# Kernel tuning notes

Hardware: AMD Instinct MI355X
Metric: run time of the kernel (lower is better)

Reference implementation:

```python
import jax, jax.numpy as jnp
import numpy as np

B, S, HID = 2, 2048, 3072
NH, NKV, HD = 16, 8, 256
N_REP = NH // NKV
BITS, BLK = 4, 128
THETA = 10000.0
NEG = -1e9


def quantize_bfp(x, bits=BITS, block_size=BLK):
    """Block-floating-point quantization: blocks of `block_size` along the last
    (head_dim) axis share one power-of-two exponent; mantissas get `bits` levels
    (sign + bits-1), round-to-nearest."""
    shape = x.shape
    xb = x.reshape(-1, block_size)
    maxabs = jnp.max(jnp.abs(xb), axis=-1, keepdims=True)
    e = jnp.floor(jnp.log2(jnp.maximum(maxabs, 1e-30)))
    scale = jnp.exp2(e - (bits - 2))  # largest mantissa ~ 2^(bits-1)-1 covers maxabs
    qmax = 2.0 ** (bits - 1) - 1.0
    q = jnp.clip(jnp.round(xb / scale), -qmax, qmax) * scale
    q = jnp.where(maxabs > 0, q, 0.0)
    return q.reshape(shape)


def rotate_half(x):
    x1, x2 = jnp.split(x, 2, axis=-1)
    return jnp.concatenate((-x2, x1), axis=-1)


def setup_inputs() -> dict:
    key = jax.random.key(0)
    ks = jax.random.split(key, 5)
    hidden_states = jax.random.normal(ks[0], (B, S, HID), dtype=jnp.float32)
    sd = 0.02
    Wq = jax.random.normal(ks[1], (NH * HD, HID), dtype=jnp.float32) * sd
    Wk = jax.random.normal(ks[2], (NKV * HD, HID), dtype=jnp.float32) * sd
    Wv = jax.random.normal(ks[3], (NKV * HD, HID), dtype=jnp.float32) * sd
    Wo = jax.random.normal(ks[4], (HID, NH * HD), dtype=jnp.float32) * sd
    # rotary tables (HF convention: concat(freqs, freqs))
    pos = jnp.arange(S, dtype=jnp.float32)
    inv_freq = 1.0 / (THETA ** (jnp.arange(0, HD, 2, dtype=jnp.float32) / HD))
    freqs = jnp.einsum('s,d->sd', pos, inv_freq)
    emb = jnp.concatenate((freqs, freqs), axis=-1)  # (S, HD)
    cos = jnp.cos(emb)[None]  # (1, S, HD)
    sin = jnp.sin(emb)[None]
    # additive causal mask (B, 1, S, S)
    causal = jnp.where(jnp.tril(jnp.ones((S, S), dtype=bool)), 0.0, NEG).astype(jnp.float32)
    attention_mask = jnp.broadcast_to(causal[None, None], (B, 1, S, S))
    return {"hidden_states": hidden_states, "Wq": Wq, "Wk": Wk, "Wv": Wv,
            "Wo": Wo, "cos": cos, "sin": sin, "attention_mask": attention_mask}


def reference(hidden_states, Wq, Wk, Wv, Wo, cos, sin, attention_mask):
    b, s, _ = hidden_states.shape
    q = jnp.einsum('bsh,dh->bsd', hidden_states, Wq).reshape(b, s, NH, HD).transpose(0, 2, 1, 3)
    k = jnp.einsum('bsh,dh->bsd', hidden_states, Wk).reshape(b, s, NKV, HD).transpose(0, 2, 1, 3)
    v = jnp.einsum('bsh,dh->bsd', hidden_states, Wv).reshape(b, s, NKV, HD).transpose(0, 2, 1, 3)
    # RoPE (cos/sin unsqueezed at dim 1 -> (1,1,S,HD))
    c, sn = cos[:, None], sin[:, None]
    q = q * c + rotate_half(q) * sn
    k = k * c + rotate_half(k) * sn
    # int4 BFP quantization of keys (along rows of head_dim)
    k = quantize_bfp(k)
    # GQA: repeat kv heads
    k = jnp.repeat(k, N_REP, axis=1)
    v = jnp.repeat(v, N_REP, axis=1)
    scores = jnp.einsum('bhqd,bhkd->bhqk', q, k) / jnp.sqrt(jnp.float32(HD))
    scores = scores + attention_mask
    attn = jax.nn.softmax(scores.astype(jnp.float32), axis=-1).astype(q.dtype)
    out = jnp.einsum('bhqk,bhkd->bhqd', attn, v)
    out = out.transpose(0, 2, 1, 3).reshape(b, s, NH * HD)
    return jnp.einsum('bsd,hd->bsh', out, Wo)
```

## Files before the change

### kernel.cpp

```cpp
#include <hip/hip_runtime.h>
#include <math.h>

#define Bsz 2
#define Ssz 2048
#define HIDs 3072
#define NHs 16
#define NKVs 8
#define HDs 256

typedef _Float16 f16;
typedef _Float16 f16x8 __attribute__((ext_vector_type(8)));
typedef _Float16 f16x4 __attribute__((ext_vector_type(4)));
typedef float f32x4 __attribute__((ext_vector_type(4)));

__device__ __forceinline__ void async16(const f16* g, f16* l) {
    __builtin_amdgcn_global_load_lds(
        (const __attribute__((address_space(1))) void*)g,
        (__attribute__((address_space(3))) void*)l, 16, 0, 0);
}

__device__ __forceinline__ float row_max16(float v) {
    int t;
    t = __builtin_amdgcn_mov_dpp(__float_as_int(v), 0x121, 0xf, 0xf, false);
    v = fmaxf(v, __int_as_float(t));
    t = __builtin_amdgcn_mov_dpp(__float_as_int(v), 0x122, 0xf, 0xf, false);
    v = fmaxf(v, __int_as_float(t));
    t = __builtin_amdgcn_mov_dpp(__float_as_int(v), 0x124, 0xf, 0xf, false);
    v = fmaxf(v, __int_as_float(t));
    t = __builtin_amdgcn_mov_dpp(__float_as_int(v), 0x128, 0xf, 0xf, false);
    v = fmaxf(v, __int_as_float(t));
    return v;
}
__device__ __forceinline__ float row_sum16(float v) {
    int t;
    t = __builtin_amdgcn_mov_dpp(__float_as_int(v), 0x121, 0xf, 0xf, false);
    v = v + __int_as_float(t);
    t = __builtin_amdgcn_mov_dpp(__float_as_int(v), 0x122, 0xf, 0xf, false);
    v = v + __int_as_float(t);
    t = __builtin_amdgcn_mov_dpp(__float_as_int(v), 0x124, 0xf, 0xf, false);
    v = v + __int_as_float(t);
    t = __builtin_amdgcn_mov_dpp(__float_as_int(v), 0x128, 0xf, 0xf, false);
    v = v + __int_as_float(t);
    return v;
}

__global__ void cast_f32_f16_v4(const float4* __restrict__ in, f16x4* __restrict__ out, int n4) {
    int i = blockIdx.x * blockDim.x + threadIdx.x;
    if (i < n4) {
        float4 v = in[i];
        f16x4 r;
        r[0] = (f16)v.x; r[1] = (f16)v.y; r[2] = (f16)v.z; r[3] = (f16)v.w;
        out[i] = r;
    }
}

__global__ __launch_bounds__(256) void gemm_nt_f16(
    const f16* __restrict__ A, const f16* __restrict__ Bm, float* __restrict__ C,
    int M, int N, int K)
{
    __shared__ __align__(16) f16 As[128 * 32];
    __shared__ __align__(16) f16 Bs[128 * 32];
    const int tid  = threadIdx.x;
    const int wave = tid >> 6, lane = tid & 63;
    const int l15  = lane & 15, quad = lane >> 4;
    const int m0 = blockIdx.y * 128, n0 = blockIdx.x * 128;
    const int wm = (wave >> 1) * 64, wn = (wave & 1) * 64;
    const int srow = wave * 32 + (lane >> 2);
    const int scol = (lane & 3) * 8;

    f32x4 acc[4][4];
    const f32x4 fz = {0.f, 0.f, 0.f, 0.f};
#pragma unroll
    for (int i = 0; i < 4; i++)
#pragma unroll
        for (int j = 0; j < 4; j++) acc[i][j] = fz;

    const f16* Ag0 = A  + (size_t)(m0 + srow) * K + scol;
    const f16* Ag1 = A  + (size_t)(m0 + srow + 16) * K + scol;
    const f16* Bg0 = Bm + (size_t)(n0 + srow) * K + scol;
    const f16* Bg1 = Bm + (size_t)(n0 + srow + 16) * K + scol;
    f16* Al0 = As + (wave * 32) * 32;
    f16* Al1 = As + (wave * 32 + 16) * 32;
    f16* Bl0 = Bs + (wave * 32) * 32;
    f16* Bl1 = Bs + (wave * 32 + 16) * 32;

    for (int k0 = 0; k0 < K; k0 += 32) {
        __syncthreads();
        async16(Ag0 + k0, Al0);
        async16(Ag1 + k0, Al1);
        async16(Bg0 + k0, Bl0);
        async16(Bg1 + k0, Bl1);
        __syncthreads();
        f16x8 af[4], bfr[4];
#pragma unroll
        for (int i = 0; i < 4; i++)
            af[i] = *(const f16x8*)(As + (wm + i * 16 + l15) * 32 + quad * 8);
#pragma unroll
        for (int j = 0; j < 4; j++)
            bfr[j] = *(const f16x8*)(Bs + (wn + j * 16 + l15) * 32 + quad * 8);
#pragma unroll
        for (int i = 0; i < 4; i++)
#pragma unroll
            for (int j = 0; j < 4; j++)
                acc[i][j] = __builtin_amdgcn_mfma_f32_16x16x32_f16(af[i], bfr[j], acc[i][j], 0, 0, 0);
    }
#pragma unroll
    for (int i = 0; i < 4; i++) {
        const int r = m0 + wm + i * 16 + quad * 4;
#pragma unroll
        for (int j = 0; j < 4; j++) {
            const int c = n0 + wn + j * 16 + l15;
#pragma unroll
            for (int rr = 0; rr < 4; rr++)
                C[(size_t)(r + rr) * N + c] = acc[i][j][rr];
        }
    }
}

__global__ void rope_q_kernel(const float* __restrict__ qp, const float* __restrict__ cosb,
                              const float* __restrict__ sinb, f16* __restrict__ qo) {
    const int s = blockIdx.x, h = blockIdx.y, b = blockIdx.z;
    const int d = threadIdx.x;
    const float* row = qp + (size_t)(b * Ssz + s) * (NHs * HDs) + h * HDs;
    float x = row[d];
    float other = (d < 128) ? -row[d + 128] : row[d - 128];
    float val = (x * cosb[s * HDs + d] + other * sinb[s * HDs + d]) * 0.0625f;
    qo[((size_t)(b * NHs + h) * Ssz + s) * HDs + d] = (f16)val;
}

__global__ void rope_quant_k_kernel(const float* __restrict__ kp, const float* __restrict__ cosb,
                                    const float* __restrict__ sinb, f16* __restrict__ ko) {
    const int s = blockIdx.x, h = blockIdx.y, b = blockIdx.z;
    const int d = threadIdx.x;
    const float* row = kp + (size_t)(b * Ssz + s) * (NKVs * HDs) + h * HDs;
    float x = row[d];
    float other = (d < 128) ? -row[d + 128] : row[d - 128];
    float val = x * cosb[s * HDs + d] + other * sinb[s * HDs + d];
    __shared__ float red[256];
    red[d] = fabsf(val);
    __syncthreads();
    for (int off = 64; off >= 1; off >>= 1) {
        if ((d & 127) < off) red[d] = fmaxf(red[d], red[d + off]);
        __syncthreads();
    }
    float maxabs = red[d & 128];
    float out;
    if (maxabs > 0.f) {
        int ex;
        frexpf(maxabs, &ex);
        float scale = ldexpf(1.0f, ex - 3);
        float q = rintf(val / scale);
        q = fminf(7.f, fmaxf(-7.f, q));
        out = q * scale;
    } else out = 0.f;
    ko[((size_t)(b * NKVs + h) * Ssz + s) * HDs + d] = (f16)out;
}

__global__ __launch_bounds__(256) void transpose_v_kernel(
    const float* __restrict__ proj, f16* __restrict__ vt)
{
    const int s0 = blockIdx.x * 64, c0 = blockIdx.y * 64, b = blockIdx.z;
    const int tid = threadIdx.x;
    __shared__ f16 T[64 * 72];
    {
        const int r = tid >> 2, cc = (tid & 3) * 16;
        const float* src = proj + (size_t)(b * Ssz + s0 + r) * (NKVs * HDs) + c0 + cc;
        f16 tmp[16];
#pragma unroll
        for (int q4 = 0; q4 < 4; q4++) {
            float4 v = *(const float4*)(src + q4 * 4);
            tmp[q4 * 4 + 0] = (f16)v.x; tmp[q4 * 4 + 1] = (f16)v.y;
            tmp[q4 * 4 + 2] = (f16)v.z; tmp[q4 * 4 + 3] = (f16)v.w;
        }
        *(f16x8*)(T + r * 72 + cc)     = *(f16x8*)(tmp);
        *(f16x8*)(T + r * 72 + cc + 8) = *(f16x8*)(tmp + 8);
    }
    __syncthreads();
    {
        const int d = tid >> 2, sc = (tid & 3) * 16;
        f16 tmp[16];
#pragma unroll
        for (int j = 0; j < 16; j++) tmp[j] = T[(sc + j) * 72 + d];
        const int col = c0 + d;
        const int kh = col >> 8, dd = col & 255;
        f16* dst = vt + ((size_t)(b * NKVs + kh) * HDs + dd) * Ssz + s0 + sc;
        *(f16x8*)(dst)     = *(f16x8*)(tmp);
        *(f16x8*)(dst + 8) = *(f16x8*)(tmp + 8);
    }
}

__global__ __launch_bounds__(256, 2) void attn_kernel(
    const f16* __restrict__ Q,
    const f16* __restrict__ Kq,
    const f16* __restrict__ Vt,
    f16* __restrict__ O)
{
    const int qt = (gridDim.x - 1) - blockIdx.x;
    const int h = blockIdx.y, b = blockIdx.z;
    const int kh = h >> 1;
    const int tid = threadIdx.x;
    const int wave = tid >> 6, lane = tid & 63;
    const int l15 = lane & 15, quad = lane >> 4;
    const int wrow = qt * 64 + wave * 16;

    const f16* Qb  = Q  + ((size_t)(b * NHs  + h)  * Ssz) * HDs;
    const f16* Kg  = Kq + ((size_t)(b * NKVs + kh) * Ssz) * HDs;
    const f16* Vtg = Vt + ((size_t)(b * NKVs + kh) * HDs) * Ssz;

    __shared__ __align__(16) f16 Ks[32 * 256];
    __shared__ __align__(16) f16 Vs[256 * 32];
    __shared__ __align__(16) f16 Pl[4 * 16 * 40];
    f16* Pw = Pl + wave * 16 * 40;

    const int k_r   = lane >> 5;
    const int k_cs  = (lane & 31) ^ (k_r << 2);
    const int v_r   = lane >> 2;
    const int v_c   = (lane & 3) * 8;

    f16x8 qf[8];
    {
        const f16* qrow = Qb + (size_t)(wrow + l15) * HDs + quad * 8;
#pragma unroll
        for (int ks = 0; ks < 8; ks++)
            qf[ks] = *(const f16x8*)(qrow + ks * 32);
    }

    const f32x4 fz = {0.f, 0.f, 0.f, 0.f};
    f32x4 accO[16];
#pragma unroll
    for (int jn = 0; jn < 16; jn++) accO[jn] = fz;
    float mrow[4], lpart[4];
#pragma unroll
    for (int r = 0; r < 4; r++) { mrow[r] = -1e30f; lpart[r] = 0.f; }

    const int nk = 2 * qt + 2;
    const int wave_max_row = wrow + 15;

    for (int kt = 0; kt < nk; kt++) {
        const int kvb = kt * 32;
        __syncthreads();
#pragma unroll
        for (int t = 0; t < 4; t++) {
            const int r2 = wave * 8 + t * 2;
            async16(Kg + (size_t)(kvb + r2 + k_r) * 256 + k_cs * 8, Ks + r2 * 256);
        }
#pragma unroll
        for (int t = 0; t < 4; t++) {
            const int d0 = wave * 64 + t * 16;
            async16(Vtg + (size_t)(d0 + v_r) * Ssz + kvb + v_c, Vs + d0 * 32);
        }
        __syncthreads();

        if (kvb <= wave_max_row) {
            f32x4 sv0 = fz, sv1 = fz;
            const int sw0 = (l15 & 1) << 2;
#pragma unroll
            for (int ks = 0; ks < 8; ks++) {
                const int cpos = ((ks * 4 + quad) ^ sw0) * 8;
                f16x8 kf0 = *(const f16x8*)(Ks + l15 * 256 + cpos);
                f16x8 kf1 = *(const f16x8*)(Ks + (16 + l15) * 256 + cpos);
                sv0 = __builtin_amdgcn_mfma_f32_16x16x32_f16(qf[ks], kf0, sv0, 0, 0, 0);
                sv1 = __builtin_amdgcn_mfma_f32_16x16x32_f16(qf[ks], kf1, sv1, 0, 0, 0);
            }
            float aup[4];
            bool need = false;
#pragma unroll
            for (int r = 0; r < 4; r++) {
                float s0 = sv0[r], s1 = sv1[r];
                const int row = wrow + quad * 4 + r;
                if (kvb + 31 > row) {
                    if (kvb + l15 > row)      s0 = -1e30f;
                    if (kvb + 16 + l15 > row) s1 = -1e30f;
                }
                float rmax = row_max16(fmaxf(s0, s1));
                float mold = mrow[r];
                float mnew = fmaxf(mold, rmax);
                aup[r] = __expf(mold - mnew);
                need = need || (mnew > mold);
                float p0 = __expf(s0 - mnew);
                float p1 = __expf(s1 - mnew);
                lpart[r] = lpart[r] * aup[r] + (p0 + p1);
                mrow[r] = mnew;
                Pw[(quad * 4 + r) * 40 + l15]      = (f16)p0;
                Pw[(quad * 4 + r) * 40 + 16 + l15] = (f16)p1;
            }
            if (__any(need)) {
#pragma unroll
                for (int jn = 0; jn < 16; jn++) {
                    f32x4 t = accO[jn];
                    t[0] *= aup[0]; t[1] *= aup[1]; t[2] *= aup[2]; t[3] *= aup[3];
                    accO[jn] = t;
                }
            }
            f16x8 pf = *(const f16x8*)(Pw + l15 * 40 + quad * 8);
#pragma unroll
            for (int jn = 0; jn < 16; jn++) {
                f16x8 vf = *(const f16x8*)(Vs + (jn * 16 + l15) * 32 + quad * 8);
                accO[jn] = __builtin_amdgcn_mfma_f32_16x16x32_f16(pf, vf, accO[jn], 0, 0, 0);
            }
        }
    }
#pragma unroll
    for (int r = 0; r < 4; r++) {
        const int row = wrow + quad * 4 + r;
        const float inv = 1.0f / row_sum16(lpart[r]);
        f16* orow = O + ((size_t)(b * Ssz) + row) * (NHs * HDs) + h * HDs;
#pragma unroll
        for (int jn = 0; jn < 16; jn++)
            orow[jn * 16 + l15] = (f16)(accO[jn][r] * inv);
    }
}

extern "C" void kernel_launch(void* const* d_in, const int* in_sizes, int n_in,
                              void* d_out, int out_size, void* d_ws, size_t ws_size,
                              hipStream_t stream) {
    const float* hs   = (const float*)d_in[0];
    const float* Wq   = (const float*)d_in[1];
    const float* Wk   = (const float*)d_in[2];
    const float* Wv   = (const float*)d_in[3];
    const float* Wo   = (const float*)d_in[4];
    const float* cosb = (const float*)d_in[5];
    const float* sinb = (const float*)d_in[6];
    float* out = (float*)d_out;

    char* ws = (char*)d_ws;
    f16*   hs_h = (f16*)(ws);
    f16*   w_h  = (f16*)(ws + 25165824);
    float* proj = (float*)(ws + 50331648);
    f16*   q_h  = (f16*)(ws + 117440512);
    f16*   k_h  = (f16*)(ws + 150994944);
    f16*   vt_h = (f16*)(ws + 167772160);
    f16*   ao_h = (f16*)proj;

    int n4;
    n4 = (Bsz * Ssz * HIDs) / 4;
    cast_f32_f16_v4<<<n4 / 256, 256, 0, stream>>>((const float4*)hs, (f16x4*)hs_h, n4);
    n4 = (NHs * HDs * HIDs) / 4;
    cast_f32_f16_v4<<<n4 / 256, 256, 0, stream>>>((const float4*)Wq, (f16x4*)w_h, n4);
    gemm_nt_f16<<<dim3(4096 / 128, 4096 / 128), 256, 0, stream>>>(hs_h, w_h, proj, 4096, 4096, 3072);
    rope_q_kernel<<<dim3(Ssz, NHs, Bsz), 256, 0, stream>>>(proj, cosb, sinb, q_h);
    n4 = (NKVs * HDs * HIDs) / 4;
    cast_f32_f16_v4<<<n4 / 256, 256, 0, stream>>>((const float4*)Wk, (f16x4*)w_h, n4);
    gemm_nt_f16<<<dim3(2048 / 128, 4096 / 128), 256, 0, stream>>>(hs_h, w_h, proj, 4096, 2048, 3072);
    rope_quant_k_kernel<<<dim3(Ssz, NKVs, Bsz), 256, 0, stream>>>(proj, cosb, sinb, k_h);
    n4 = (NKVs * HDs * HIDs) / 4;
    cast_f32_f16_v4<<<n4 / 256, 256, 0, stream>>>((const float4*)Wv, (f16x4*)w_h, n4);
    gemm_nt_f16<<<dim3(2048 / 128, 4096 / 128), 256, 0, stream>>>(hs_h, w_h, proj, 4096, 2048, 3072);
    transpose_v_kernel<<<dim3(Ssz / 64, (NKVs * HDs) / 64, Bsz), 256, 0, stream>>>(proj, vt_h);
    attn_kernel<<<dim3(Ssz / 64, NHs, Bsz), 256, 0, stream>>>(q_h, k_h, vt_h, ao_h);
    n4 = (HIDs * NHs * HDs) / 4;
    cast_f32_f16_v4<<<n4 / 256, 256, 0, stream>>>((const float4*)Wo, (f16x4*)w_h, n4);
    gemm_nt_f16<<<dim3(3072 / 128, 4096 / 128), 256, 0, stream>>>(ao_h, w_h, out, 4096, 3072, 4096);
}
```

Before: 1.021 ms.

## Double-buffer K/V tiles in LDS to overlap async loads with MFMA compute

Splits the K and V shared-memory tiles into two buffers and issues the async global-to-LDS loads for the next KV tile before computing on the current one. Raw s_barrier and s_waitcnt vmcnt calls replace the two __syncthreads per iteration, so only the older batch of loads must land before each barrier. This is meant to hide global load latency behind the QK and PV MFMAs. The cost is doubled LDS (about 69KB per block), which may prevent two blocks per CU, and the hand-written waitcnt encodings must correctly cover the loads each wave issued.

```diff
diff --git a/kernel.cpp b/kernel.cpp
--- a/kernel.cpp
+++ b/kernel.cpp
@@ -207,8 +207,8 @@
     const f16* Kg  = Kq + ((size_t)(b * NKVs + kh) * Ssz) * HDs;
     const f16* Vtg = Vt + ((size_t)(b * NKVs + kh) * HDs) * Ssz;
 
-    __shared__ __align__(16) f16 Ks[32 * 256];
-    __shared__ __align__(16) f16 Vs[256 * 32];
+    __shared__ __align__(16) f16 Ks[2][32 * 256];
+    __shared__ __align__(16) f16 Vs[2][256 * 32];
     __shared__ __align__(16) f16 Pl[4 * 16 * 40];
     f16* Pw = Pl + wave * 16 * 40;
 
@@ -236,29 +236,45 @@
     const int nk = 2 * qt + 2;
     const int wave_max_row = wrow + 15;
 
-    for (int kt = 0; kt < nk; kt++) {
+    auto stage = [&](int kt, int bi) {
         const int kvb = kt * 32;
-        __syncthreads();
+        f16* KsB = &Ks[bi][0];
+        f16* VsB = &Vs[bi][0];
 #pragma unroll
         for (int t = 0; t < 4; t++) {
             const int r2 = wave * 8 + t * 2;
-            async16(Kg + (size_t)(kvb + r2 + k_r) * 256 + k_cs * 8, Ks + r2 * 256);
+            async16(Kg + (size_t)(kvb + r2 + k_r) * 256 + k_cs * 8, KsB + r2 * 256);
         }
 #pragma unroll
         for (int t = 0; t < 4; t++) {
             const int d0 = wave * 64 + t * 16;
-            async16(Vtg + (size_t)(d0 + v_r) * Ssz + kvb + v_c, Vs + d0 * 32);
-        }
-        __syncthreads();
-
+            async16(Vtg + (size_t)(d0 + v_r) * Ssz + kvb + v_c, VsB + d0 * 32);
+        }
+    };
+
+    stage(0, 0);
+    for (int kt = 0; kt < nk; kt++) {
+        const int cur = kt & 1;
+        if (kt + 1 < nk) {
+            if (kt >= 1) __builtin_amdgcn_s_barrier();
+            stage(kt + 1, cur ^ 1);
+            __builtin_amdgcn_s_waitcnt(0x0F78);
+        } else {
+            __builtin_amdgcn_s_waitcnt(0x0F70);
+        }
+        __builtin_amdgcn_s_barrier();
+
+        const int kvb = kt * 32;
         if (kvb <= wave_max_row) {
+            const f16* KsB = &Ks[cur][0];
+            const f16* VsB = &Vs[cur][0];
             f32x4 sv0 = fz, sv1 = fz;
             const int sw0 = (l15 & 1) << 2;
 #pragma unroll
             for (int ks = 0; ks < 8; ks++) {
                 const int cpos = ((ks * 4 + quad) ^ sw0) * 8;
-                f16x8 kf0 = *(const f16x8*)(Ks + l15 * 256 + cpos);
-                f16x8 kf1 = *(const f16x8*)(Ks + (16 + l15) * 256 + cpos);
+                f16x8 kf0 = *(const f16x8*)(KsB + l15 * 256 + cpos);
+                f16x8 kf1 = *(const f16x8*)(KsB + (16 + l15) * 256 + cpos);
                 sv0 = __builtin_amdgcn_mfma_f32_16x16x32_f16(qf[ks], kf0, sv0, 0, 0, 0);
                 sv1 = __builtin_amdgcn_mfma_f32_16x16x32_f16(qf[ks], kf1, sv1, 0, 0, 0);
             }
@@ -295,7 +311,7 @@
             f16x8 pf = *(const f16x8*)(Pw + l15 * 40 + quad * 8);
 #pragma unroll
             for (int jn = 0; jn < 16; jn++) {
-                f16x8 vf = *(const f16x8*)(Vs + (jn * 16 + l15) * 32 + quad * 8);
+                f16x8 vf = *(const f16x8*)(VsB + (jn * 16 + l15) * 32 + quad * 8);
                 accO[jn] = __builtin_amdgcn_mfma_f32_16x16x32_f16(pf, vf, accO[jn], 0, 0, 0);
             }
         }
```

Result: no change. 1.026 ms (+0.5%).
